# Kernel tuning notes

Hardware: AMD Instinct MI355X
Metric: run time of the kernel (lower is better)

## Reference

```python
import jax, jax.numpy as jnp
import numpy as np

N_SPECIES = 4
HIDDEN = 256
SILU_GAIN = 1.6765  # normalization constant for SiLU (1/sqrt(E[silu(x)^2]) for x~N(0,1))
AVG_N_ATOMS = 64.0  # average_number_of_atoms from the training set


def _norm_linear(x, w):
    # normalize_func('linear_no_bias', Linear): bias-free linear scaled by 1/sqrt(fan_in)
    return (x @ w) * (1.0 / np.sqrt(w.shape[0]))


def _norm_silu(x):
    # normalize_func('activation', SiLU): variance-preserving SiLU
    return jax.nn.silu(x) * SILU_GAIN


def _species_mlp(x, w1, w2, w3, w4):
    h = _norm_silu(_norm_linear(x, w1))
    h = _norm_silu(_norm_linear(h, w2))
    h = _norm_silu(_norm_linear(h, w3))
    return _norm_linear(h, w4)[:, 0]  # [n_atoms]


def setup_inputs() -> dict:
    key = jax.random.key(0)
    ks = jax.random.split(key, 8)
    n_atoms, n_feat, n_structures = 32768, 1920, 512
    features = jax.random.normal(ks[0], (n_atoms, n_feat), dtype=jnp.float32)
    species = jax.random.randint(ks[1], (n_atoms,), 0, N_SPECIES)
    structure_indices = jnp.sort(jax.random.randint(ks[2], (n_atoms,), 0, n_structures))
    W1 = jax.random.normal(ks[3], (N_SPECIES, n_feat, HIDDEN), dtype=jnp.float32)
    W2 = jax.random.normal(ks[4], (N_SPECIES, HIDDEN, HIDDEN), dtype=jnp.float32)
    W3 = jax.random.normal(ks[5], (N_SPECIES, HIDDEN, HIDDEN), dtype=jnp.float32)
    W4 = jax.random.normal(ks[6], (N_SPECIES, HIDDEN, 1), dtype=jnp.float32)
    composition_coefficients = jax.random.normal(ks[7], (N_SPECIES,), dtype=jnp.float32)
    return {
        "features": features,
        "W1": W1, "W2": W2, "W3": W3, "W4": W4,
        "composition_coefficients": composition_coefficients,
        "species": species,
        "structure_indices": structure_indices,
        "n_structures": n_structures,
    }


def reference(features, W1, W2, W3, W4, composition_coefficients,
              species, structure_indices, n_structures):
    # Per-species MLP heads (loop over the small, fixed species set; jit-friendly
    # replacement for ragged per-center_type gather blocks).
    per_species = jnp.stack(
        [_species_mlp(features, W1[s], W2[s], W3[s], W4[s]) for s in range(N_SPECIES)],
        axis=0,
    )  # [S, n_atoms]
    atomic_energies = jnp.take_along_axis(per_species, species[None, :], axis=0)[0]
    # energies.index_add_ over structure index
    energies = jax.ops.segment_sum(atomic_energies, structure_indices,
                                   num_segments=n_structures)
    energies = energies * (AVG_N_ATOMS ** -0.5)
    # composition term: per-structure species counts @ coefficients
    onehot = jax.nn.one_hot(species, N_SPECIES, dtype=features.dtype)
    comp = jax.ops.segment_sum(onehot, structure_indices, num_segments=n_structures)
    energies = energies + comp @ composition_coefficients
    return energies
```

## Files before the change

kernel.cpp:

```cpp
#include <hip/hip_runtime.h>

#define NATOMS 32768
#define NFEAT 1920
#define HIDDEN 256
#define NSPEC 4
#define NSTRUCT 512
#define BK 32
#define MT128 260
#define MPAD (MT128 * 128)
#define NT1 (NFEAT / BK)
#define NBLK1 (MT128 * 2)
#define NBLK2 ((MPAD / 64) * 2)

typedef __bf16 bf16x8 __attribute__((ext_vector_type(8)));
typedef float f32x4 __attribute__((ext_vector_type(4)));
typedef float f4v __attribute__((ext_vector_type(4)));
typedef unsigned short us4 __attribute__((ext_vector_type(4)));

#define WS_INTS 0
#define WS_PERM 256
#define WS_W1T (WS_PERM + MPAD * 4)
#define WS_W2T WS_W1T
#define WS_W3T (WS_W2T + NSPEC * HIDDEN * HIDDEN * 2)
#define WS_W4T (WS_W1T + NSPEC * HIDDEN * NFEAT * 2)
#define WS_H1  (WS_W4T + 4096)
#define WS_H2  (WS_H1 + (size_t)MPAD * HIDDEN * 2)

__device__ __forceinline__ unsigned short f2bf(float f) {
  unsigned int u = __float_as_uint(f);
  u += 0x7fffu + ((u >> 16) & 1u);
  return (unsigned short)(u >> 16);
}
__device__ __forceinline__ float bf2f(unsigned short s) {
  return __uint_as_float(((unsigned int)s) << 16);
}
__device__ __forceinline__ float silu_n(float x) {
  return (x / (1.f + __expf(-x))) * 1.6765f;
}

__device__ __forceinline__ void gll16(const void* g, void* l) {
  __builtin_amdgcn_global_load_lds(
      (const __attribute__((address_space(1))) void*)g,
      (__attribute__((address_space(3))) void*)l, 16, 0, 0);
}


__global__ void k_init(int* ints, int* perm, float* out) {
  int i = blockIdx.x * blockDim.x + threadIdx.x;
  if (i < MPAD) perm[i] = -1;
  if (i < NSTRUCT) out[i] = 0.f;
  if (i < 8) ints[i] = 0;
  if (i >= 32 && i < 48) ((float*)ints)[i] = 0.f;
}

__global__ void k_count(const int* __restrict__ species, int* counts) {
  __shared__ int c[NSPEC];
  int tid = threadIdx.x;
  if (tid < NSPEC) c[tid] = 0;
  __syncthreads();
  int s = species[blockIdx.x * 256 + tid];
  int lane = tid & 63;
#pragma unroll
  for (int sp = 0; sp < NSPEC; ++sp) {
    unsigned long long m = __ballot(s == sp);
    if (lane == 0 && m) atomicAdd(&c[sp], __popcll(m));
  }
  __syncthreads();
  if (tid < NSPEC && c[tid]) atomicAdd(&counts[tid], c[tid]);
}

__global__ void k_offsets(int* ints) {
  int* counts = ints;
  int* cursors = ints + 4;
  int* off = ints + 8;
  off[0] = 0;
  for (int s = 0; s < NSPEC; ++s) {
    off[s + 1] = off[s] + ((counts[s] + 127) & ~127);
    cursors[s] = off[s];
  }
}

__global__ void k_scatter(const int* __restrict__ species, int* ints, int* perm) {
  __shared__ int cnt[4][NSPEC];
  __shared__ int base[NSPEC];
  int tid = threadIdx.x;
  int w = tid >> 6, lane = tid & 63;
  int i = blockIdx.x * 256 + tid;
  int s = species[i];
  unsigned long long m0 = __ballot(s == 0);
  unsigned long long m1 = __ballot(s == 1);
  unsigned long long m2 = __ballot(s == 2);
  unsigned long long m3 = __ballot(s == 3);
  if (lane == 0) {
    cnt[w][0] = __popcll(m0);
    cnt[w][1] = __popcll(m1);
    cnt[w][2] = __popcll(m2);
    cnt[w][3] = __popcll(m3);
  }
  __syncthreads();
  if (tid < NSPEC) {
    int t = cnt[0][tid] + cnt[1][tid] + cnt[2][tid] + cnt[3][tid];
    base[tid] = t ? atomicAdd(&ints[4 + tid], t) : 0;
  }
  __syncthreads();
  unsigned long long mm = (s == 0) ? m0 : (s == 1) ? m1 : (s == 2) ? m2 : m3;
  int pos = base[s] + __popcll(mm & ((1ull << lane) - 1ull));
#pragma unroll
  for (int ww = 0; ww < 4; ++ww)
    if (ww < w) pos += cnt[ww][s];
  perm[pos] = i;
}

__global__ void k_wtile(const float* __restrict__ src, unsigned short* __restrict__ dst,
                        int K, int N) {
  __shared__ unsigned short T[64][72];
  int ntN = N >> 6, ntK = K >> 6;
  int per = ntK * ntN;
  int b = blockIdx.x;
  int s = b / per, rem = b % per;
  int k0 = (rem / ntN) << 6;
  int n0 = (rem % ntN) << 6;
  int tid = threadIdx.x;
  int r = tid >> 2, cb = (tid & 3) << 4;
  const float* p = src + ((size_t)s * K + k0 + r) * N + n0 + cb;
#pragma unroll
  for (int j = 0; j < 16; j += 4) {
    f4v v = *(const f4v*)(p + j);
#pragma unroll
    for (int e = 0; e < 4; ++e) T[r][cb + j + e] = f2bf(v[e]);
  }
  __syncthreads();
  unsigned short* base = dst + (size_t)s * HIDDEN * K;
  int row_n = n0 + r;
#pragma unroll
  for (int g2 = 0; g2 < 2; ++g2) {
    int kl = cb + g2 * 8;
    int kg = k0 + kl;
    int t = kg >> 5;
    int kgl = (kg >> 3) & 3;
    int lanepos = ((row_n & 15) << 2) | (kgl ^ ((row_n >> 2) & 3));
    unsigned short v[8];
#pragma unroll
    for (int e = 0; e < 8; ++e) v[e] = T[kl + e][r];
    uint4 u;
    u.x = v[0] | ((unsigned)v[1] << 16);
    u.y = v[2] | ((unsigned)v[3] << 16);
    u.z = v[4] | ((unsigned)v[5] << 16);
    u.w = v[6] | ((unsigned)v[7] << 16);
    *(uint4*)(base + (size_t)t * 8192 + ((row_n >> 4) << 9) + lanepos * 8) = u;
  }
}

__global__ void k_w4(const float* __restrict__ src, unsigned short* __restrict__ dst) {
  int i = blockIdx.x * 256 + threadIdx.x;
  dst[i] = f2bf(src[i]);
}

__global__ __launch_bounds__(512) void k_l1n(
    const float* __restrict__ xf, const unsigned short* __restrict__ Wt,
    unsigned short* __restrict__ Hout, const int* __restrict__ perm,
    const int* __restrict__ off, const float* __restrict__ zs, float scale) {
  __shared__ __align__(16) unsigned short Asl[2 * 8192];
  __shared__ __align__(16) unsigned short Bsl[2 * 4096];
  float* af = (float*)Asl;
  unsigned short* bl = Bsl;

  int nwg = gridDim.x;
  int xcd = blockIdx.x & 7, idx = blockIdx.x >> 3;
  int q = nwg >> 3, r = nwg & 7;
  int lb = (xcd < r ? xcd * (q + 1) : r * (q + 1) + (xcd - r) * q) + idx;
  int mt = lb >> 1, bn = lb & 1;

  int rowbase = mt * 128;
  int tid = threadIdx.x;
  int w = tid >> 6, lane = tid & 63;
  int wr = w >> 1, wc = w & 1;
  int lr = lane & 15, lg = lane >> 4;

  int sp;
  if (rowbase < off[1]) sp = 0;
  else if (rowbase < off[2]) sp = 1;
  else if (rowbase < off[3]) sp = 2;
  else sp = 3;

  const float* srcA[2];
  int ldsA[2];
#pragma unroll
  for (int qq = 0; qq < 2; ++qq) {
    int c = qq * 8 + w;
    int row = c * 8 + (lane >> 3);
    int slot = (lane & 7) ^ (row & 7);
    long as = perm[rowbase + row];
    srcA[qq] = (as >= 0) ? (xf + (size_t)as * NFEAT + slot * 4) : nullptr;
    ldsA[qq] = c * 256;
  }
  const unsigned short* wsp =
      Wt + (size_t)sp * HIDDEN * NFEAT + (size_t)bn * 4096;

  auto STAGE = [&](int b, int t) {
#pragma unroll
    for (int qq = 0; qq < 2; ++qq) {
      const float* s = srcA[qq] ? srcA[qq] + t * BK : zs;
      gll16(s, af + b * 4096 + ldsA[qq]);
    }
    gll16(wsp + (size_t)t * 8192 + tid * 8, bl + b * 4096 + tid * 8);
  };

  f32x4 zero4 = {0.f, 0.f, 0.f, 0.f};
  f32x4 acc[2][4];
#pragma unroll
  for (int m = 0; m < 2; ++m)
#pragma unroll
    for (int n = 0; n < 4; ++n) acc[m][n] = zero4;

  STAGE(0, 0);
  __syncthreads();
  int buf = 0;
  for (int t = 0; t < NT1; ++t) {
    if (t + 1 < NT1) STAGE(buf ^ 1, t + 1);

    bf16x8 a[2], b[4];
#pragma unroll
    for (int m = 0; m < 2; ++m) {
      int row = wr * 32 + m * 16 + lr;
      const float* base = af + buf * 4096 + row * 32;
      f4v x0 = *(const f4v*)(base + (((lg << 1) ^ (row & 7)) << 2));
      f4v x1 = *(const f4v*)(base + ((((lg << 1) | 1) ^ (row & 7)) << 2));
      unsigned r01, r23, r45, r67;
      asm("v_cvt_pk_bf16_f32 %0, %1, %2" : "=v"(r01) : "v"(x0[0]), "v"(x0[1]));
      asm("v_cvt_pk_bf16_f32 %0, %1, %2" : "=v"(r23) : "v"(x0[2]), "v"(x0[3]));
      asm("v_cvt_pk_bf16_f32 %0, %1, %2" : "=v"(r45) : "v"(x1[0]), "v"(x1[1]));
      asm("v_cvt_pk_bf16_f32 %0, %1, %2" : "=v"(r67) : "v"(x1[2]), "v"(x1[3]));
      union { unsigned u[4]; bf16x8 v; } cv = {{r01, r23, r45, r67}};
      a[m] = cv.v;
    }
#pragma unroll
    for (int n = 0; n < 4; ++n) {
      int row = wc * 64 + n * 16 + lr;
      b[n] = *(const bf16x8*)(bl + buf * 4096 + row * 32 +
                              ((lg ^ ((row >> 2) & 3)) << 3));
    }
#pragma unroll
    for (int m = 0; m < 2; ++m)
#pragma unroll
      for (int n = 0; n < 4; ++n)
        acc[m][n] = __builtin_amdgcn_mfma_f32_16x16x32_bf16(a[m], b[n], acc[m][n], 0, 0, 0);

    __syncthreads();
    buf ^= 1;
  }

#pragma unroll
  for (int m = 0; m < 2; ++m)
#pragma unroll
    for (int n = 0; n < 4; ++n)
#pragma unroll
      for (int rr = 0; rr < 4; ++rr) {
        float v = acc[m][n][rr] * scale;
        Hout[(size_t)(rowbase + wr * 32 + m * 16 + lg * 4 + rr) * HIDDEN +
             bn * 128 + wc * 64 + n * 16 + lr] = f2bf(silu_n(v));
      }
}

__global__ __launch_bounds__(256) void k_mlp2(
    const unsigned short* __restrict__ xb, const unsigned short* __restrict__ Wt,
    unsigned short* __restrict__ Hout, const int* __restrict__ off, float scale) {
  constexpr int K = HIDDEN;
  __shared__ __align__(16) unsigned short Asl[2 * 2048];
  __shared__ __align__(16) unsigned short Bsl[2 * 4096];
  unsigned short* ab = Asl;
  unsigned short* bl = Bsl;

  int nwg = gridDim.x;
  int xcd = blockIdx.x & 7, idx = blockIdx.x >> 3;
  int q = nwg >> 3, r = nwg & 7;
  int lb = (xcd < r ? xcd * (q + 1) : r * (q + 1) + (xcd - r) * q) + idx;
  int mt = lb >> 1, bn = lb & 1;

  int rowbase = mt * 64;
  int tid = threadIdx.x;
  int w = tid >> 6, lane = tid & 63;
  int wr = w >> 1, wc = w & 1;
  int lr = lane & 15, lg = lane >> 4;

  int sp;
  if (rowbase < off[1]) sp = 0;
  else if (rowbase < off[2]) sp = 1;
  else if (rowbase < off[3]) sp = 2;
  else sp = 3;

  const unsigned short* srcB[2];
  int ldsB[2];
#pragma unroll
  for (int qq = 0; qq < 2; ++qq) {
    int gc = bn * 8 + w * 2 + qq;
    srcB[qq] = Wt + (size_t)sp * HIDDEN * K + gc * 512 + lane * 8;
    ldsB[qq] = (w * 2 + qq) * 512;
  }
  int arow = w * 16 + (lane >> 2);
  int aslot = (lane & 3) ^ ((arow >> 2) & 3);
  const unsigned short* srcA1 = xb + ((size_t)(rowbase + arow)) * K + aslot * 8;
  int ldsA1 = w * 512;

  auto STAGE = [&](int b, int t) {
    gll16(srcA1 + t * BK, ab + b * 2048 + ldsA1);
#pragma unroll
    for (int qq = 0; qq < 2; ++qq)
      gll16(srcB[qq] + (size_t)t * 8192, bl + b * 4096 + ldsB[qq]);
  };

  f32x4 zero4 = {0.f, 0.f, 0.f, 0.f};
  f32x4 acc[2][4];
#pragma unroll
  for (int m = 0; m < 2; ++m)
#pragma unroll
    for (int n = 0; n < 4; ++n) acc[m][n] = zero4;

  constexpr int NT = K / BK;
  STAGE(0, 0);
  __syncthreads();
  int buf = 0;
  for (int t = 0; t < NT; ++t) {
    if (t + 1 < NT) STAGE(buf ^ 1, t + 1);

    bf16x8 a[2], b[4];
#pragma unroll
    for (int m = 0; m < 2; ++m) {
      int row = wr * 32 + m * 16 + lr;
      a[m] = *(const bf16x8*)(ab + buf * 2048 + row * 32 +
                              ((lg ^ ((row >> 2) & 3)) << 3));
    }
#pragma unroll
    for (int n = 0; n < 4; ++n) {
      int row = wc * 64 + n * 16 + lr;
      b[n] = *(const bf16x8*)(bl + buf * 4096 + row * 32 +
                              ((lg ^ ((row >> 2) & 3)) << 3));
    }
#pragma unroll
    for (int m = 0; m < 2; ++m)
#pragma unroll
      for (int n = 0; n < 4; ++n)
        acc[m][n] = __builtin_amdgcn_mfma_f32_16x16x32_bf16(a[m], b[n], acc[m][n], 0, 0, 0);

    __syncthreads();
    buf ^= 1;
  }

#pragma unroll
  for (int m = 0; m < 2; ++m)
#pragma unroll
    for (int n = 0; n < 4; ++n)
#pragma unroll
      for (int rr = 0; rr < 4; ++rr) {
        float v = acc[m][n][rr] * scale;
        Hout[(size_t)(rowbase + wr * 32 + m * 16 + lg * 4 + rr) * HIDDEN +
             bn * 128 + wc * 64 + n * 16 + lr] = f2bf(silu_n(v));
      }
}

__global__ void k_l4(const unsigned short* __restrict__ H3, const unsigned short* __restrict__ W4t,
                     const int* __restrict__ perm, const int* __restrict__ species,
                     const int* __restrict__ sidx, const float* __restrict__ coeff,
                     float* __restrict__ out) {
  int w = threadIdx.x >> 6, l = threadIdx.x & 63;
  int row = blockIdx.x * 4 + w;
  int src = perm[row];
  if (src < 0) return;
  int sp = species[src];
  us4 h = *(const us4*)&H3[(size_t)row * HIDDEN + l * 4];
  us4 wv = *(const us4*)&W4t[sp * HIDDEN + l * 4];
  float sum = 0.f;
#pragma unroll
  for (int e = 0; e < 4; ++e) sum += bf2f(h[e]) * bf2f(wv[e]);
#pragma unroll
  for (int d = 32; d >= 1; d >>= 1) sum += __shfl_xor(sum, d, 64);
  if (l == 0)
    atomicAdd(&out[sidx[src]], sum * (0.0625f * 0.125f) + coeff[sp]);
}

extern "C" void kernel_launch(void* const* d_in, const int* in_sizes, int n_in,
                              void* d_out, int out_size, void* d_ws, size_t ws_size,
                              hipStream_t stream) {
  const float* features = (const float*)d_in[0];
  const float* W1 = (const float*)d_in[1];
  const float* W2 = (const float*)d_in[2];
  const float* W3 = (const float*)d_in[3];
  const float* W4 = (const float*)d_in[4];
  const float* coeff = (const float*)d_in[5];
  const int* species = (const int*)d_in[6];
  const int* sidx = (const int*)d_in[7];
  float* out = (float*)d_out;

  char* ws = (char*)d_ws;
  int* ints = (int*)(ws + WS_INTS);
  const float* zs = (const float*)(ws + 128);
  int* perm = (int*)(ws + WS_PERM);
  unsigned short* W1t = (unsigned short*)(ws + WS_W1T);
  unsigned short* W2t = (unsigned short*)(ws + WS_W2T);
  unsigned short* W3t = (unsigned short*)(ws + WS_W3T);
  unsigned short* W4t = (unsigned short*)(ws + WS_W4T);
  unsigned short* H1 = (unsigned short*)(ws + WS_H1);
  unsigned short* H2 = (unsigned short*)(ws + WS_H2);

  k_init<<<(MPAD + 255) / 256, 256, 0, stream>>>(ints, perm, out);
  k_count<<<NATOMS / 256, 256, 0, stream>>>(species, ints);
  k_offsets<<<1, 1, 0, stream>>>(ints);
  k_scatter<<<NATOMS / 256, 256, 0, stream>>>(species, ints, perm);

  k_wtile<<<NSPEC * (NFEAT / 64) * (HIDDEN / 64), 256, 0, stream>>>(W1, W1t, NFEAT, HIDDEN);
  k_w4<<<NSPEC, 256, 0, stream>>>(W4, W4t);

  const float s1 = 1.f / sqrtf((float)NFEAT);
  const float s2 = 1.f / 16.f;

  k_l1n<<<NBLK1, 512, 0, stream>>>(features, W1t, H1, perm, ints + 8, zs, s1);

  k_wtile<<<NSPEC * (HIDDEN / 64) * (HIDDEN / 64), 256, 0, stream>>>(W2, W2t, HIDDEN, HIDDEN);
  k_wtile<<<NSPEC * (HIDDEN / 64) * (HIDDEN / 64), 256, 0, stream>>>(W3, W3t, HIDDEN, HIDDEN);

  k_mlp2<<<NBLK2, 256, 0, stream>>>(H1, W2t, H2, ints + 8, s2);
  k_mlp2<<<NBLK2, 256, 0, stream>>>(H2, W3t, H1, ints + 8, s2);

  k_l4<<<MPAD / 4, 256, 0, stream>>>(H1, W4t, perm, species, sidx, coeff, out);
}
```

Baseline: 169.2 us.

## Split layer-1 GEMM over K halves with full-N tiles and a combine kernel

Layer-1 now gives each block all 256 output columns for a 128-row tile but only half of the 1920-long K dimension. Each half writes a partial sum to its own bf16 buffer, and a new elementwise kernel adds the two halves and applies SiLU. Before, each block covered half of N, so every block loaded the full fp32 feature row tile, which means the large features matrix was read twice. The change is meant to remove that duplicate read. In exchange it adds partial-sum round-trips through memory, an extra launch, bf16 rounding of the partial sums, and more accumulator registers per wave.

```diff
diff --git a/kernel.cpp b/kernel.cpp
--- a/kernel.cpp
+++ b/kernel.cpp
@@ -8,7 +8,8 @@
 #define BK 32
 #define MT128 260
 #define MPAD (MT128 * 128)
-#define NT1 (NFEAT / BK)
+#define KC2 960
+#define NT1 (KC2 / BK)
 #define NBLK1 (MT128 * 2)
 #define NBLK2 ((MPAD / 64) * 2)
 
@@ -16,6 +17,7 @@
 typedef float f32x4 __attribute__((ext_vector_type(4)));
 typedef float f4v __attribute__((ext_vector_type(4)));
 typedef unsigned short us4 __attribute__((ext_vector_type(4)));
+typedef unsigned short us8 __attribute__((ext_vector_type(8)));
 
 #define WS_INTS 0
 #define WS_PERM 256
@@ -25,6 +27,9 @@
 #define WS_W4T (WS_W1T + NSPEC * HIDDEN * NFEAT * 2)
 #define WS_H1  (WS_W4T + 4096)
 #define WS_H2  (WS_H1 + (size_t)MPAD * HIDDEN * 2)
+#define WS_HP0 (WS_H2 + (size_t)MPAD * HIDDEN * 2)
+#define WS_HP1 (WS_HP0 + (size_t)MPAD * HIDDEN * 2)
+#define WS_END (WS_HP1 + (size_t)MPAD * HIDDEN * 2)
 
 __device__ __forceinline__ unsigned short f2bf(float f) {
   unsigned int u = __float_as_uint(f);
@@ -156,12 +161,13 @@
   dst[i] = f2bf(src[i]);
 }
 
-__global__ __launch_bounds__(512) void k_l1n(
+__global__ __launch_bounds__(512) void k_l1p(
     const float* __restrict__ xf, const unsigned short* __restrict__ Wt,
-    unsigned short* __restrict__ Hout, const int* __restrict__ perm,
-    const int* __restrict__ off, const float* __restrict__ zs, float scale) {
+    unsigned short* __restrict__ Hp0, unsigned short* __restrict__ Hp1,
+    const int* __restrict__ perm, const int* __restrict__ off,
+    const float* __restrict__ zs, float scale) {
   __shared__ __align__(16) unsigned short Asl[2 * 8192];
-  __shared__ __align__(16) unsigned short Bsl[2 * 4096];
+  __shared__ __align__(16) unsigned short Bsl[2 * 8192];
   float* af = (float*)Asl;
   unsigned short* bl = Bsl;
 
@@ -169,12 +175,13 @@
   int xcd = blockIdx.x & 7, idx = blockIdx.x >> 3;
   int q = nwg >> 3, r = nwg & 7;
   int lb = (xcd < r ? xcd * (q + 1) : r * (q + 1) + (xcd - r) * q) + idx;
-  int mt = lb >> 1, bn = lb & 1;
+  int kc = lb / MT128;
+  int mt = lb % MT128;
 
   int rowbase = mt * 128;
   int tid = threadIdx.x;
   int w = tid >> 6, lane = tid & 63;
-  int wr = w >> 1, wc = w & 1;
+  int wr = w >> 2, wc = w & 3;
   int lr = lane & 15, lg = lane >> 4;
 
   int sp;
@@ -191,11 +198,19 @@
     int row = c * 8 + (lane >> 3);
     int slot = (lane & 7) ^ (row & 7);
     long as = perm[rowbase + row];
-    srcA[qq] = (as >= 0) ? (xf + (size_t)as * NFEAT + slot * 4) : nullptr;
+    srcA[qq] = (as >= 0) ? (xf + (size_t)as * NFEAT + kc * KC2 + slot * 4) : nullptr;
     ldsA[qq] = c * 256;
   }
   const unsigned short* wsp =
-      Wt + (size_t)sp * HIDDEN * NFEAT + (size_t)bn * 4096;
+      Wt + (size_t)sp * HIDDEN * NFEAT + (size_t)(kc * NT1) * 8192;
+  const unsigned short* srcB[2];
+  int ldsB[2];
+#pragma unroll
+  for (int qq = 0; qq < 2; ++qq) {
+    int c = qq * 8 + w;
+    srcB[qq] = wsp + c * 512 + lane * 8;
+    ldsB[qq] = c * 512;
+  }
 
   auto STAGE = [&](int b, int t) {
 #pragma unroll
@@ -203,13 +218,15 @@
       const float* s = srcA[qq] ? srcA[qq] + t * BK : zs;
       gll16(s, af + b * 4096 + ldsA[qq]);
     }
-    gll16(wsp + (size_t)t * 8192 + tid * 8, bl + b * 4096 + tid * 8);
+#pragma unroll
+    for (int qq = 0; qq < 2; ++qq)
+      gll16(srcB[qq] + (size_t)t * 8192, bl + b * 8192 + ldsB[qq]);
   };
 
   f32x4 zero4 = {0.f, 0.f, 0.f, 0.f};
-  f32x4 acc[2][4];
-#pragma unroll
-  for (int m = 0; m < 2; ++m)
+  f32x4 acc[4][4];
+#pragma unroll
+  for (int m = 0; m < 4; ++m)
 #pragma unroll
     for (int n = 0; n < 4; ++n) acc[m][n] = zero4;
 
@@ -219,10 +236,10 @@
   for (int t = 0; t < NT1; ++t) {
     if (t + 1 < NT1) STAGE(buf ^ 1, t + 1);
 
-    bf16x8 a[2], b[4];
-#pragma unroll
-    for (int m = 0; m < 2; ++m) {
-      int row = wr * 32 + m * 16 + lr;
+    bf16x8 a[4], b[4];
+#pragma unroll
+    for (int m = 0; m < 4; ++m) {
+      int row = wr * 64 + m * 16 + lr;
       const float* base = af + buf * 4096 + row * 32;
       f4v x0 = *(const f4v*)(base + (((lg << 1) ^ (row & 7)) << 2));
       f4v x1 = *(const f4v*)(base + ((((lg << 1) | 1) ^ (row & 7)) << 2));
@@ -237,11 +254,11 @@
 #pragma unroll
     for (int n = 0; n < 4; ++n) {
       int row = wc * 64 + n * 16 + lr;
-      b[n] = *(const bf16x8*)(bl + buf * 4096 + row * 32 +
+      b[n] = *(const bf16x8*)(bl + buf * 8192 + row * 32 +
                               ((lg ^ ((row >> 2) & 3)) << 3));
     }
 #pragma unroll
-    for (int m = 0; m < 2; ++m)
+    for (int m = 0; m < 4; ++m)
 #pragma unroll
       for (int n = 0; n < 4; ++n)
         acc[m][n] = __builtin_amdgcn_mfma_f32_16x16x32_bf16(a[m], b[n], acc[m][n], 0, 0, 0);
@@ -250,16 +267,28 @@
     buf ^= 1;
   }
 
-#pragma unroll
-  for (int m = 0; m < 2; ++m)
+  unsigned short* Hp = kc ? Hp1 : Hp0;
+#pragma unroll
+  for (int m = 0; m < 4; ++m)
 #pragma unroll
     for (int n = 0; n < 4; ++n)
 #pragma unroll
-      for (int rr = 0; rr < 4; ++rr) {
-        float v = acc[m][n][rr] * scale;
-        Hout[(size_t)(rowbase + wr * 32 + m * 16 + lg * 4 + rr) * HIDDEN +
-             bn * 128 + wc * 64 + n * 16 + lr] = f2bf(silu_n(v));
-      }
+      for (int rr = 0; rr < 4; ++rr)
+        Hp[(size_t)(rowbase + wr * 64 + m * 16 + lg * 4 + rr) * HIDDEN +
+           wc * 64 + n * 16 + lr] = f2bf(acc[m][n][rr] * scale);
+}
+
+__global__ void k_comb(const unsigned short* __restrict__ hp0,
+                       const unsigned short* __restrict__ hp1,
+                       unsigned short* __restrict__ h1) {
+  size_t i = ((size_t)blockIdx.x * 256 + threadIdx.x) * 8;
+  us8 a = *(const us8*)(hp0 + i);
+  us8 b = *(const us8*)(hp1 + i);
+  us8 o;
+#pragma unroll
+  for (int e = 0; e < 8; ++e)
+    o[e] = f2bf(silu_n(bf2f(a[e]) + bf2f(b[e])));
+  *(us8*)(h1 + i) = o;
 }
 
 __global__ __launch_bounds__(256) void k_mlp2(
@@ -401,6 +430,8 @@
   unsigned short* W4t = (unsigned short*)(ws + WS_W4T);
   unsigned short* H1 = (unsigned short*)(ws + WS_H1);
   unsigned short* H2 = (unsigned short*)(ws + WS_H2);
+  unsigned short* Hp0 = (unsigned short*)(ws + WS_HP0);
+  unsigned short* Hp1 = (unsigned short*)(ws + WS_HP1);
 
   k_init<<<(MPAD + 255) / 256, 256, 0, stream>>>(ints, perm, out);
   k_count<<<NATOMS / 256, 256, 0, stream>>>(species, ints);
@@ -413,11 +444,13 @@
   const float s1 = 1.f / sqrtf((float)NFEAT);
   const float s2 = 1.f / 16.f;
 
-  k_l1n<<<NBLK1, 512, 0, stream>>>(features, W1t, H1, perm, ints + 8, zs, s1);
+  k_l1p<<<NBLK1, 512, 0, stream>>>(features, W1t, Hp0, Hp1, perm, ints + 8, zs, s1);
 
   k_wtile<<<NSPEC * (HIDDEN / 64) * (HIDDEN / 64), 256, 0, stream>>>(W2, W2t, HIDDEN, HIDDEN);
   k_wtile<<<NSPEC * (HIDDEN / 64) * (HIDDEN / 64), 256, 0, stream>>>(W3, W3t, HIDDEN, HIDDEN);
 
+  k_comb<<<(MPAD * HIDDEN) / (256 * 8), 256, 0, stream>>>(Hp0, Hp1, H1);
+
   k_mlp2<<<NBLK2, 256, 0, stream>>>(H1, W2t, H2, ints + 8, s2);
   k_mlp2<<<NBLK2, 256, 0, stream>>>(H2, W3t, H1, ints + 8, s2);
 
```

Result: slower. 193.1 us (+14.1%).
